# Kernel optimization log

Measured on AMD Instinct MI355X. Metric: run time of the kernel, lower is better.

## Reference

```python
import jax, jax.numpy as jnp
import numpy as np


def _sqdist(X1, X2):
    # squared euclidean distance matrix, matches torch.cdist(...,p=2)**2
    d2 = (jnp.sum(X1 * X1, -1)[:, None] + jnp.sum(X2 * X2, -1)[None, :]
          - 2.0 * (X1 @ X2.T))
    return jnp.maximum(d2, 0.0)


def setup_inputs() -> dict:
    key = jax.random.key(0)
    k1, k2, k3, k4, k5, k6 = jax.random.split(key, 6)
    n, m, d, C = 1024, 2048, 4, 64
    X_train = jax.random.normal(k1, (n, d), dtype=jnp.float32)
    y_train = jax.random.normal(k2, (n,), dtype=jnp.float32)
    X_test = jax.random.normal(k3, (m, d), dtype=jnp.float32)
    # positive params within the priors' supports
    lengthscale = jax.random.uniform(k4, (C,), minval=0.1, maxval=3.0, dtype=jnp.float32)
    variance = jax.random.uniform(k5, (C,), minval=0.1, maxval=3.0, dtype=jnp.float32)
    noise = jax.random.uniform(k6, (C,), minval=0.01, maxval=0.5, dtype=jnp.float32)
    return {"X_train": X_train, "y_train": y_train, "X_test": X_test,
            "lengthscale": lengthscale, "variance": variance, "noise": noise}


def reference(X_train, y_train, X_test, lengthscale, variance, noise):
    n = X_train.shape[0]
    ls2 = (lengthscale ** 2)[:, None, None]          # [C,1,1]
    var = variance[:, None, None]                     # [C,1,1]
    d2_tr = _sqdist(X_train, X_train)                 # [n,n]
    d2_te = _sqdist(X_test, X_train)                  # [m,n]
    K_train = var * jnp.exp(-0.5 * d2_tr[None] / ls2)   # [C,n,n]
    K_test = var * jnp.exp(-0.5 * d2_te[None] / ls2)    # [C,m,n]
    K_noisy = K_train + noise[:, None, None] * jnp.eye(n, dtype=K_train.dtype)
    L = jnp.linalg.cholesky(K_noisy)                  # batched [C,n,n]

    def per_chain(Lc, Ktc):
        solve = jax.scipy.linalg.solve_triangular
        z = solve(Lc, y_train, lower=True)            # [n]
        alpha = solve(Lc, z, lower=True, trans=1)     # [n]
        pred_mean = Ktc @ alpha                       # [m]
        v = solve(Lc, Ktc.T, lower=True)              # [n,m]
        pred_var = jnp.sum(v * v, axis=0)             # [m]
        return pred_mean, pred_var

    means, vars_ = jax.vmap(per_chain)(L, K_test)     # [C,m] each
    return means.mean(axis=0), vars_.mean(axis=0)
```

## Files before the change

### kernel.cpp

```cpp
#include <hip/hip_runtime.h>
#include <hip/hip_fp16.h>
#include <math.h>

#define N 1024
#define M 2048
#define C 64
#define NB 128
#define TB 8
#define NBLK 36
#define PL ((size_t)NBLK*NB*NB)

typedef __attribute__((ext_vector_type(8))) short bf16x8;
typedef __attribute__((ext_vector_type(8))) _Float16 f16x8;
typedef __attribute__((ext_vector_type(4))) float f32x4;

__device__ __forceinline__ size_t pblk(int ib, int jt){
    return ((size_t)((ib*(ib+1))/2 + jt))*((size_t)NB*NB);
}

#define TT(r,c) T[(r)][(((c)+(r)) & 127)]


__device__ __forceinline__ float sqdist4(const float4 a, const float4 b){
    float dx=a.x-b.x, dy=a.y-b.y, dz=a.z-b.z, dw=a.w-b.w;
    return dx*dx+dy*dy+dz*dz+dw*dw;
}

__device__ __forceinline__ void split4(float x0, float x1, float x2, float x3,
                                       uint2& hi, uint2& lo){
    unsigned b0=__float_as_uint(x0), b1=__float_as_uint(x1),
             b2=__float_as_uint(x2), b3=__float_as_uint(x3);
    unsigned h0=b0&0xFFFF0000u, h1=b1&0xFFFF0000u, h2=b2&0xFFFF0000u, h3=b3&0xFFFF0000u;
    hi.x = (h0>>16)|h1;  hi.y = (h2>>16)|h3;
    float l0=x0-__uint_as_float(h0), l1=x1-__uint_as_float(h1),
          l2=x2-__uint_as_float(h2), l3=x3-__uint_as_float(h3);
    lo.x = (__float_as_uint(l0)>>16) | (__float_as_uint(l1)&0xFFFF0000u);
    lo.y = (__float_as_uint(l2)>>16) | (__float_as_uint(l3)&0xFFFF0000u);
}

__device__ void chol_invert_lds(float T[NB][NB], int tid){
    for (int j = 0; j < NB; j++){
        float d = TT(j,j);
        float inv = 1.0f / sqrtf(d);
        for (int i = j+1+tid; i < NB; i += 256) TT(i,j) *= inv;
        if (tid == 0) TT(j,j) = d * inv;
        __syncthreads();
        int i = j+1 + (tid >> 1);
        if (i < NB){
            float lij = TT(i,j);
            for (int k = j+1+(tid&1); k <= i; k += 2)
                TT(i,k) -= lij * TT(k,j);
        }
        __syncthreads();
    }
    for (int i = 0; i < NB; i++){
        float inv_ii = 1.0f / TT(i,i);
        int j = tid & 127, hi = tid >> 7;
        float S = 0.0f;
        if (j < i){
            for (int k = i-1-hi; k >= j; k -= 2)
                S += TT(i,k) * TT(k,j);
        }
        if (hi && j < i) TT(j,i) = S;
        __syncthreads();
        if (!hi){
            if (j < i)      TT(i,j) = -inv_ii * (S + TT(j,i));
            else if (j == i) TT(i,i) = inv_ii;
        }
        __syncthreads();
    }
}


struct FragLds { __half Ah[4096], Al[4096], Bh[4096], Bl[4096]; };

__device__ __forceinline__ void stage_f16(__half* __restrict__ Hh, __half* __restrict__ Hl,
                                          const float* __restrict__ S, int ld,
                                          int k0, bool contig, int tid){
    #pragma unroll
    for (int h = 0; h < 2; h++){
        int u = tid + h*256;
        int fr = u & 15, kg = (u>>4)&3, rt = (u>>6)&3, hf = u>>8;
        int rc = hf*64 + rt*16 + fr;
        int kk = k0 + kg*8;
        float x[8];
        if (contig){
            float4 v0 = *(const float4*)&S[(size_t)rc*ld + kk];
            float4 v1 = *(const float4*)&S[(size_t)rc*ld + kk + 4];
            x[0]=v0.x;x[1]=v0.y;x[2]=v0.z;x[3]=v0.w;
            x[4]=v1.x;x[5]=v1.y;x[6]=v1.z;x[7]=v1.w;
        } else {
            #pragma unroll
            for (int e=0;e<8;e++) x[e] = S[(size_t)(kk+e)*ld + rc];
        }
        union { __half h[8]; uint4 u4; } Hi, Lo;
        #pragma unroll
        for (int e=0;e<8;e++){
            __half hv = __float2half_rn(x[e]);
            Hi.h[e] = hv;
            Lo.h[e] = __float2half_rn(x[e] - __half2float(hv));
        }
        *(uint4*)&Hh[(size_t)u*8] = Hi.u4;
        *(uint4*)&Hl[(size_t)u*8] = Lo.u4;
    }
}

__device__ __forceinline__ void mfma_slab_f16(const __half* Ah, const __half* Al,
                                              const __half* Bh, const __half* Bl,
                                              int wrow, int wcol, int lane,
                                              f32x4 acc[4][4]){
    f16x8 ah[4], al[4];
    #pragma unroll
    for (int rt=0;rt<4;rt++){
        ah[rt] = *(const f16x8*)&Ah[((size_t)((wrow*4+rt)*64 + lane))*8];
        al[rt] = *(const f16x8*)&Al[((size_t)((wrow*4+rt)*64 + lane))*8];
    }
    #pragma unroll
    for (int ct=0;ct<4;ct++){
        f16x8 bh = *(const f16x8*)&Bh[((size_t)((wcol*4+ct)*64 + lane))*8];
        f16x8 bl = *(const f16x8*)&Bl[((size_t)((wcol*4+ct)*64 + lane))*8];
        #pragma unroll
        for (int rt=0;rt<4;rt++){
            f32x4 a = acc[rt][ct];
            a = __builtin_amdgcn_mfma_f32_16x16x32_f16(ah[rt], bh, a, 0,0,0);
            a = __builtin_amdgcn_mfma_f32_16x16x32_f16(ah[rt], bl, a, 0,0,0);
            a = __builtin_amdgcn_mfma_f32_16x16x32_f16(al[rt], bh, a, 0,0,0);
            acc[rt][ct] = a;
        }
    }
}

__device__ void gemm_f16_unit(const float* __restrict__ A, int lda,
                              const float* __restrict__ B, int ldb, bool bContig,
                              FragLds& F, f32x4 acc[4][4], int tid){
    int lane = tid & 63, w = tid >> 6, wrow = w>>1, wcol = w&1;
    for (int k0 = 0; k0 < NB; k0 += 32){
        __syncthreads();
        stage_f16(F.Ah, F.Al, A, lda, k0, true, tid);
        stage_f16(F.Bh, F.Bl, B, ldb, k0, bContig, tid);
        __syncthreads();
        mfma_slab_f16(F.Ah, F.Al, F.Bh, F.Bl, wrow, wcol, lane, acc);
    }
}

__device__ __forceinline__ void store_f16acc(float* __restrict__ Cp, int ldc,
                                             const f32x4 acc[4][4], float sgn, int tid){
    int lane = tid&63, w = tid>>6, wrow = w>>1, wcol = w&1;
    int fr = lane&15, kg = lane>>4;
    #pragma unroll
    for (int rt=0;rt<4;rt++)
      #pragma unroll
      for (int ct=0;ct<4;ct++)
        #pragma unroll
        for (int r=0;r<4;r++){
            int row = wrow*64 + rt*16 + kg*4 + r;
            int col = wcol*64 + ct*16 + fr;
            Cp[(size_t)row*ldc + col] = sgn*acc[rt][ct][r];
        }
}

#define ZERO_ACC(acc) { _Pragma("unroll") for (int zi=0;zi<4;zi++) _Pragma("unroll") for (int zj=0;zj<4;zj++) acc[zi][zj] = (f32x4)0.0f; }


__global__ void k_init_acc(float* __restrict__ acc){
    int i = blockIdx.x*blockDim.x + threadIdx.x;
    if (i < 2*M) acc[i] = 0.0f;
}

__global__ void k_build_d2te(const float* __restrict__ Xtr, const float* __restrict__ Xte,
                             float* __restrict__ d2){
    int j = blockIdx.x;
    float4 xj = ((const float4*)Xte)[j];
    for (int i = threadIdx.x; i < N; i += blockDim.x){
        float4 xi = ((const float4*)Xtr)[i];
        d2[(size_t)j*N + i] = sqdist4(xi,xj);
    }
}

__global__ __launch_bounds__(256) void k_build_K(const float* __restrict__ Xtr,
                          const float* __restrict__ ls,
                          const float* __restrict__ var, const float* __restrict__ noise,
                          float* __restrict__ Lbuf){
    __shared__ float4 xr[NB], xc[NB];
    int c = blockIdx.y, flat = blockIdx.x;
    int ib = 0; while ((ib+1)*(ib+2)/2 <= flat) ib++;
    int jt = flat - ib*(ib+1)/2;
    int tid = threadIdx.x;
    if (tid < NB) xr[tid] = ((const float4*)Xtr)[ib*NB + tid];
    else          xc[tid-NB] = ((const float4*)Xtr)[jt*NB + (tid-NB)];
    __syncthreads();
    float il2 = 1.0f/(ls[c]*ls[c]);
    float vc = var[c], nc = noise[c];
    float* blk = Lbuf + c*PL + pblk(ib,jt);
    for (int idx = tid; idx < NB*NB; idx += 256){
        int r = idx >> 7, col = idx & 127;
        float d2v = sqdist4(xr[r], xc[col]);
        float v = vc*__expf(-0.5f*d2v*il2);
        if (ib==jt && r==col) v += nc;
        blk[idx] = v;
    }
}

__global__ __launch_bounds__(256) void k_diagF(float* __restrict__ Lbuf){
    __shared__ float T[NB][NB];
    int c = blockIdx.x, tid = threadIdx.x;
    float* A = Lbuf + c*PL + pblk(0,0);
    for (int idx = tid; idx < NB*NB; idx += 256){
        int r = idx >> 7, col = idx & 127;
        TT(r,col) = A[idx];
    }
    __syncthreads();
    chol_invert_lds(T, tid);
    for (int idx = tid; idx < NB*NB; idx += 256){
        int r = idx >> 7, col = idx & 127;
        A[idx] = (col <= r) ? TT(r,col) : 0.0f;
    }
}

__global__ __launch_bounds__(256) void k_panel(float* __restrict__ Lbuf, int kb){
    __shared__ FragLds F;
    int c = blockIdx.x;
    int ib = kb + 1 + blockIdx.y;
    int tid = threadIdx.x;
    float* base = Lbuf + c*PL;
    float* Ablk = base + pblk(ib,kb);
    const float* Dv = base + pblk(kb,kb);
    f32x4 acc[4][4]; ZERO_ACC(acc);
    gemm_f16_unit(Ablk, NB, Dv, NB, true, F, acc, tid);
    store_f16acc(Ablk, NB, acc, 1.0f, tid);
}

union SmU2 { FragLds f; float T[NB][NB]; };
__global__ __launch_bounds__(256) void k_syrk(float* __restrict__ Lbuf, int kb){
    __shared__ SmU2 sm;
    int c = blockIdx.x;
    int flat = blockIdx.y;
    int di = 0; while ((di+1)*(di+2)/2 <= flat) di++;
    int dj = flat - di*(di+1)/2;
    int i = kb+1+di, j = kb+1+dj;
    int tid = threadIdx.x;
    float* base = Lbuf + c*PL;
    float* Cblk = base + pblk(i,j);
    const float* Ablk = base + pblk(i,kb);
    const float* Bblk = base + pblk(j,kb);
    f32x4 acc[4][4]; ZERO_ACC(acc);
    gemm_f16_unit(Ablk, NB, Bblk, NB, true, sm.f, acc, tid);
    int lane = tid&63, w = tid>>6, wrow = w>>1, wcol = w&1;
    int fr = lane&15, kg = lane>>4;
    if (flat != 0){
        #pragma unroll
        for (int rt=0;rt<4;rt++)
          #pragma unroll
          for (int ct=0;ct<4;ct++)
            #pragma unroll
            for (int r=0;r<4;r++){
                int row = wrow*64 + rt*16 + kg*4 + r;
                int col = wcol*64 + ct*16 + fr;
                Cblk[(size_t)row*NB + col] -= acc[rt][ct][r];
            }
    } else {
        __syncthreads();
        float (*T)[NB] = sm.T;
        #pragma unroll
        for (int rt=0;rt<4;rt++)
          #pragma unroll
          for (int ct=0;ct<4;ct++)
            #pragma unroll
            for (int r=0;r<4;r++){
                int row = wrow*64 + rt*16 + kg*4 + r;
                int col = wcol*64 + ct*16 + fr;
                TT(row,col) = Cblk[(size_t)row*NB + col] - acc[rt][ct][r];
            }
        __syncthreads();
        chol_invert_lds(T, tid);
        for (int idx = tid; idx < NB*NB; idx += 256){
            int r = idx >> 7, col = idx & 127;
            Cblk[idx] = (col <= r) ? TT(r,col) : 0.0f;
        }
    }
}

__global__ __launch_bounds__(256) void k_gemmA(float* __restrict__ Trow,
                                               const float* __restrict__ Lbuf, int ib){
    __shared__ FragLds F;
    int c = blockIdx.x, ct = blockIdx.y;
    int tid = threadIdx.x;
    const float* base = Lbuf + c*PL;
    const float* Dv = base + pblk(ib,ib);
    const float* Bsrc = base + pblk(ib,ct);
    f32x4 acc[4][4]; ZERO_ACC(acc);
    gemm_f16_unit(Dv, NB, Bsrc, NB, false, F, acc, tid);
    store_f16acc(Trow + (size_t)c*NB*N + ct*NB, N, acc, 1.0f, tid);
}

__global__ __launch_bounds__(256) void k_gemmB(float* __restrict__ Lbuf,
                                               const float* __restrict__ Trow, int ib){
    __shared__ FragLds F;
    int c = blockIdx.x, jt = blockIdx.y;
    int tid = threadIdx.x;
    const float* G = Trow + (size_t)c*NB*N;
    float* base = Lbuf + c*PL;
    f32x4 acc[4][4]; ZERO_ACC(acc);
    for (int kt = jt; kt < ib; kt++)
        gemm_f16_unit(G + kt*NB, N, base + pblk(kt,jt), NB, false, F, acc, tid);
    store_f16acc(base + pblk(ib,jt), NB, acc, -1.0f, tid);
}

__global__ void k_zvec(const float* __restrict__ Lbuf, const float* __restrict__ y,
                       float* __restrict__ z){
    int c = blockIdx.x;
    int p = blockIdx.y * 4 + (threadIdx.x >> 6);
    int lane = threadIdx.x & 63;
    int pb = p >> 7, pl = p & 127;
    const float* base = Lbuf + c*PL;
    float s = 0.0f;
    for (int kt = 0; kt <= pb; kt++){
        const float* row = base + pblk(pb,kt) + (size_t)pl*NB;
        int lim = (kt==pb) ? pl : NB-1;
        for (int i = lane; i <= lim; i += 64) s += row[i]*y[kt*NB + i];
    }
    for (int off = 32; off; off >>= 1) s += __shfl_down(s, off);
    if (lane == 0) z[c*N + p] = s;
}

__global__ __launch_bounds__(256) void k_bigg(const float* __restrict__ Lbuf,
                                              const float* __restrict__ d2,
                                              const float* __restrict__ zbuf,
                                              const float* __restrict__ ls,
                                              const float* __restrict__ var,
                                              float* __restrict__ acc_out){
    __shared__ unsigned short Ah[4096], Al[4096], Bh[4096], Bl[4096];
    int jt = blockIdx.x, pt = blockIdx.y, c = blockIdx.z;
    int tid = threadIdx.x;
    int lane = tid & 63, w = tid >> 6;
    int wrow = w >> 1, wcol = w & 1;
    float il2 = 1.0f/(ls[c]*ls[c]);
    float vc = var[c];
    float ec = -0.5f*il2;
    const float* Arow = d2 + (size_t)(jt*NB)*N;
    const float* Wbase = Lbuf + c*PL;
    int klen = (pt+1)*NB;
    f32x4 acc[4][4]; ZERO_ACC(acc);

    int fr = lane & 15, kg = lane >> 4;

    for (int k0 = 0; k0 < klen; k0 += 32){
        const float* Bp = Wbase + pblk(pt, k0 >> 7);
        int kloc = k0 & 127;
        __syncthreads();
        #pragma unroll
        for (int h = 0; h < 2; h++){
            int u = tid + h*256;
            int ufr = u & 15, ukg = (u>>4)&3, urt = (u>>6)&3, uhf = u>>8;
            int row = uhf*64 + urt*16 + ufr;
            int kk = k0 + ukg*8;
            float4 d0 = *(const float4*)&Arow[(size_t)row*N + kk];
            float4 d1 = *(const float4*)&Arow[(size_t)row*N + kk + 4];
            float x0 = vc*__expf(ec*d0.x), x1 = vc*__expf(ec*d0.y);
            float x2 = vc*__expf(ec*d0.z), x3 = vc*__expf(ec*d0.w);
            float x4 = vc*__expf(ec*d1.x), x5 = vc*__expf(ec*d1.y);
            float x6 = vc*__expf(ec*d1.z), x7 = vc*__expf(ec*d1.w);
            uint2 h0, l0, h1, l1;
            split4(x0,x1,x2,x3, h0, l0);
            split4(x4,x5,x6,x7, h1, l1);
            *(uint4*)&Ah[(size_t)u*8] = make_uint4(h0.x,h0.y,h1.x,h1.y);
            *(uint4*)&Al[(size_t)u*8] = make_uint4(l0.x,l0.y,l1.x,l1.y);
        }
        #pragma unroll
        for (int h = 0; h < 2; h++){
            int u = tid + h*256;
            int ufr = u & 15, ukg = (u>>4)&3, urt = (u>>6)&3, uhf = u>>8;
            int p = uhf*64 + urt*16 + ufr;
            int kk = kloc + ukg*8;
            float4 w0 = *(const float4*)&Bp[(size_t)p*NB + kk];
            float4 w1 = *(const float4*)&Bp[(size_t)p*NB + kk + 4];
            uint2 h0, l0, h1, l1;
            split4(w0.x,w0.y,w0.z,w0.w, h0, l0);
            split4(w1.x,w1.y,w1.z,w1.w, h1, l1);
            *(uint4*)&Bh[(size_t)u*8] = make_uint4(h0.x,h0.y,h1.x,h1.y);
            *(uint4*)&Bl[(size_t)u*8] = make_uint4(l0.x,l0.y,l1.x,l1.y);
        }
        __syncthreads();
        bf16x8 ah[4], al[4];
        #pragma unroll
        for (int rt=0;rt<4;rt++){
            ah[rt] = *(const bf16x8*)&Ah[((size_t)((wrow*4+rt)*64 + lane))*8];
            al[rt] = *(const bf16x8*)&Al[((size_t)((wrow*4+rt)*64 + lane))*8];
        }
        #pragma unroll
        for (int ct=0;ct<4;ct++){
            bf16x8 bh = *(const bf16x8*)&Bh[((size_t)((wcol*4+ct)*64 + lane))*8];
            bf16x8 bl = *(const bf16x8*)&Bl[((size_t)((wcol*4+ct)*64 + lane))*8];
            #pragma unroll
            for (int rt=0;rt<4;rt++){
                f32x4 a = acc[rt][ct];
                a = __builtin_amdgcn_mfma_f32_16x16x32_bf16(ah[rt], bh, a, 0,0,0);
                a = __builtin_amdgcn_mfma_f32_16x16x32_bf16(ah[rt], bl, a, 0,0,0);
                a = __builtin_amdgcn_mfma_f32_16x16x32_bf16(al[rt], bh, a, 0,0,0);
                acc[rt][ct] = a;
            }
        }
    }
    float zv[4];
    #pragma unroll
    for (int ct=0;ct<4;ct++) zv[ct] = zbuf[c*N + pt*NB + wcol*64 + ct*16 + fr];
    #pragma unroll
    for (int rt=0;rt<4;rt++){
        #pragma unroll
        for (int r=0;r<4;r++){
            float m = 0.0f, v = 0.0f;
            #pragma unroll
            for (int ct=0;ct<4;ct++){
                float x = acc[rt][ct][r];
                v += x*x; m += x*zv[ct];
            }
            m += __shfl_xor(m, 1);  v += __shfl_xor(v, 1);
            m += __shfl_xor(m, 2);  v += __shfl_xor(v, 2);
            m += __shfl_xor(m, 4);  v += __shfl_xor(v, 4);
            m += __shfl_xor(m, 8);  v += __shfl_xor(v, 8);
            if (fr == 0){
                int j = jt*NB + wrow*64 + rt*16 + kg*4 + r;
                atomicAdd(&acc_out[j], m);
                atomicAdd(&acc_out[M + j], v);
            }
        }
    }
}

__global__ void k_final(const float* __restrict__ acc, float* __restrict__ out){
    int i = blockIdx.x*blockDim.x + threadIdx.x;
    if (i < 2*M) out[i] = acc[i] * (1.0f/64.0f);
}


extern "C" void kernel_launch(void* const* d_in, const int* in_sizes, int n_in,
                              void* d_out, int out_size, void* d_ws, size_t ws_size,
                              hipStream_t stream) {
    const float* Xtr = (const float*)d_in[0];
    const float* ytr = (const float*)d_in[1];
    const float* Xte = (const float*)d_in[2];
    const float* ls  = (const float*)d_in[3];
    const float* var = (const float*)d_in[4];
    const float* noi = (const float*)d_in[5];
    float* out = (float*)d_out;

    float* ws = (float*)d_ws;
    const size_t shared_fl  = (size_t)N*M + 2*M;
    const size_t perchain   = PL + (size_t)NB*N + (size_t)N;
    size_t avail = ws_size / sizeof(float);
    if (avail < shared_fl + perchain) return;
    int Gmax = (int)((avail - shared_fl) / perchain);
    if (Gmax > C) Gmax = C;
    int nbatch = (C + Gmax - 1) / Gmax;
    int G = (C + nbatch - 1) / nbatch;

    float* d2te = ws;
    float* acc  = d2te + (size_t)N*M;
    float* Lbuf = acc  + 2*M;
    float* Trow = Lbuf + (size_t)G*PL;
    float* zbuf = Trow + (size_t)G*NB*N;

    k_init_acc<<<dim3((2*M+255)/256), dim3(256), 0, stream>>>(acc);
    k_build_d2te<<<dim3(M), dim3(256), 0, stream>>>(Xtr, Xte, d2te);

    for (int c0 = 0; c0 < C; c0 += G){
        int g = C - c0 < G ? C - c0 : G;

        k_build_K<<<dim3(NBLK, g), dim3(256), 0, stream>>>(Xtr, ls+c0, var+c0, noi+c0, Lbuf);
        k_diagF<<<dim3(g), dim3(256), 0, stream>>>(Lbuf);

        for (int kb = 0; kb < TB-1; kb++){
            int rem = TB-1-kb;
            k_panel<<<dim3(g, rem), dim3(256), 0, stream>>>(Lbuf, kb);
            k_syrk<<<dim3(g, rem*(rem+1)/2), dim3(256), 0, stream>>>(Lbuf, kb);
        }
        for (int ib = 1; ib < TB; ib++){
            k_gemmA<<<dim3(g, ib), dim3(256), 0, stream>>>(Trow, Lbuf, ib);
            k_gemmB<<<dim3(g, ib), dim3(256), 0, stream>>>(Lbuf, Trow, ib);
        }
        k_zvec<<<dim3(g, N/4), dim3(256), 0, stream>>>(Lbuf, ytr, zbuf);
        k_bigg<<<dim3(M/NB, TB, g), dim3(256), 0, stream>>>(Lbuf, d2te, zbuf, ls+c0, var+c0, acc);
    }
    k_final<<<dim3((2*M+255)/256), dim3(256), 0, stream>>>(acc, out);
}
```

Before: 5.541 ms.

## Pre-split W blocks into bf16 hi/lo MFMA layout before big GEMM

Adds a kernel that converts each 128x128 fp32 block of the inverse-factor buffer in place into bf16 hi/lo halves, already arranged in the MFMA fragment order. The big GEMM then copies these images straight into shared memory instead of re-splitting fp32 values in every tile load, which removes redundant conversion work repeated across the M/NB column tiles. The A-side load is also remapped so each thread reads one coalesced float4 per row. The cost is an extra launch and pass over the buffer, and the buffer is overwritten, so any later reader of fp32 L would break.

After: 5.532 ms. About the same (-0.2%).

```diff
diff --git a/kernel.cpp b/kernel.cpp
--- a/kernel.cpp
+++ b/kernel.cpp
@@ -323,6 +323,35 @@
     if (lane == 0) z[c*N + p] = s;
 }
 
+__global__ __launch_bounds__(256) void k_wsplit(float* __restrict__ Lbuf){
+    int c = blockIdx.y, flat = blockIdx.x;
+    int tid = threadIdx.x;
+    float* blk = Lbuf + c*PL + (size_t)flat*NB*NB;
+    float4 v[16];
+    #pragma unroll
+    for (int h = 0; h < 8; h++){
+        int g = tid + h*256;
+        int u = g & 511, slab = g >> 9;
+        int fr = u&15, kg = (u>>4)&3, rt = (u>>6)&3, hf = u>>8;
+        int row = hf*64 + rt*16 + fr;
+        int k = slab*32 + kg*8;
+        v[2*h]   = *(const float4*)&blk[(size_t)row*NB + k];
+        v[2*h+1] = *(const float4*)&blk[(size_t)row*NB + k + 4];
+    }
+    __syncthreads();
+    unsigned short* out = (unsigned short*)blk;
+    #pragma unroll
+    for (int h = 0; h < 8; h++){
+        int g = tid + h*256;
+        int u = g & 511, slab = g >> 9;
+        uint2 h0, l0, h1, l1;
+        split4(v[2*h].x, v[2*h].y, v[2*h].z, v[2*h].w, h0, l0);
+        split4(v[2*h+1].x, v[2*h+1].y, v[2*h+1].z, v[2*h+1].w, h1, l1);
+        *(uint4*)&out[((size_t)(slab*2+0)*512 + u)*8] = make_uint4(h0.x,h0.y,h1.x,h1.y);
+        *(uint4*)&out[((size_t)(slab*2+1)*512 + u)*8] = make_uint4(l0.x,l0.y,l1.x,l1.y);
+    }
+}
+
 __global__ __launch_bounds__(256) void k_bigg(const float* __restrict__ Lbuf,
                                               const float* __restrict__ d2,
                                               const float* __restrict__ zbuf,
@@ -343,42 +372,31 @@
     f32x4 acc[4][4]; ZERO_ACC(acc);
 
     int fr = lane & 15, kg = lane >> 4;
+    int q = tid & 7, rs = tid >> 3;
+    int kgq = q >> 1, e4 = (q & 1) * 4;
 
     for (int k0 = 0; k0 < klen; k0 += 32){
-        const float* Bp = Wbase + pblk(pt, k0 >> 7);
-        int kloc = k0 & 127;
-        __syncthreads();
-        #pragma unroll
-        for (int h = 0; h < 2; h++){
-            int u = tid + h*256;
-            int ufr = u & 15, ukg = (u>>4)&3, urt = (u>>6)&3, uhf = u>>8;
-            int row = uhf*64 + urt*16 + ufr;
-            int kk = k0 + ukg*8;
-            float4 d0 = *(const float4*)&Arow[(size_t)row*N + kk];
-            float4 d1 = *(const float4*)&Arow[(size_t)row*N + kk + 4];
-            float x0 = vc*__expf(ec*d0.x), x1 = vc*__expf(ec*d0.y);
-            float x2 = vc*__expf(ec*d0.z), x3 = vc*__expf(ec*d0.w);
-            float x4 = vc*__expf(ec*d1.x), x5 = vc*__expf(ec*d1.y);
-            float x6 = vc*__expf(ec*d1.z), x7 = vc*__expf(ec*d1.w);
-            uint2 h0, l0, h1, l1;
-            split4(x0,x1,x2,x3, h0, l0);
-            split4(x4,x5,x6,x7, h1, l1);
-            *(uint4*)&Ah[(size_t)u*8] = make_uint4(h0.x,h0.y,h1.x,h1.y);
-            *(uint4*)&Al[(size_t)u*8] = make_uint4(l0.x,l0.y,l1.x,l1.y);
-        }
-        #pragma unroll
-        for (int h = 0; h < 2; h++){
-            int u = tid + h*256;
-            int ufr = u & 15, ukg = (u>>4)&3, urt = (u>>6)&3, uhf = u>>8;
-            int p = uhf*64 + urt*16 + ufr;
-            int kk = kloc + ukg*8;
-            float4 w0 = *(const float4*)&Bp[(size_t)p*NB + kk];
-            float4 w1 = *(const float4*)&Bp[(size_t)p*NB + kk + 4];
-            uint2 h0, l0, h1, l1;
-            split4(w0.x,w0.y,w0.z,w0.w, h0, l0);
-            split4(w1.x,w1.y,w1.z,w1.w, h1, l1);
-            *(uint4*)&Bh[(size_t)u*8] = make_uint4(h0.x,h0.y,h1.x,h1.y);
-            *(uint4*)&Bl[(size_t)u*8] = make_uint4(l0.x,l0.y,l1.x,l1.y);
+        const unsigned short* Wimg = (const unsigned short*)(Wbase + pblk(pt, k0 >> 7));
+        int slab = (k0 & 127) >> 5;
+        const unsigned short* hi_img = Wimg + (size_t)(slab*2+0)*4096;
+        const unsigned short* lo_img = Wimg + (size_t)(slab*2+1)*4096;
+        __syncthreads();
+        #pragma unroll
+        for (int p = 0; p < 4; p++){
+            int row = rs + 32*p;
+            float4 dv = *(const float4*)&Arow[(size_t)row*N + k0 + q*4];
+            float x0 = vc*__expf(ec*dv.x), x1 = vc*__expf(ec*dv.y);
+            float x2 = vc*__expf(ec*dv.z), x3 = vc*__expf(ec*dv.w);
+            uint2 hi, lo; split4(x0,x1,x2,x3, hi, lo);
+            int u = (row&15) + kgq*16 + ((row>>4)&3)*64 + (row>>6)*256;
+            *(uint2*)&Ah[(size_t)u*8 + e4] = hi;
+            *(uint2*)&Al[(size_t)u*8 + e4] = lo;
+        }
+        #pragma unroll
+        for (int h2 = 0; h2 < 2; h2++){
+            int u = tid + h2*256;
+            *(uint4*)&Bh[(size_t)u*8] = *(const uint4*)&hi_img[(size_t)u*8];
+            *(uint4*)&Bl[(size_t)u*8] = *(const uint4*)&lo_img[(size_t)u*8];
         }
         __syncthreads();
         bf16x8 ah[4], al[4];
@@ -479,6 +497,7 @@
             k_gemmB<<<dim3(g, ib), dim3(256), 0, stream>>>(Lbuf, Trow, ib);
         }
         k_zvec<<<dim3(g, N/4), dim3(256), 0, stream>>>(Lbuf, ytr, zbuf);
+        k_wsplit<<<dim3(NBLK, g), dim3(256), 0, stream>>>(Lbuf);
         k_bigg<<<dim3(M/NB, TB, g), dim3(256), 0, stream>>>(Lbuf, d2te, zbuf, ls+c0, var+c0, acc);
     }
     k_final<<<dim3((2*M+255)/256), dim3(256), 0, stream>>>(acc, out);
```
